# Kernel tuning notes

Hardware: AMD Instinct MI355X
Metric: run time of the kernel (lower is better)

Reference implementation:

```python
import jax, jax.numpy as jnp
import numpy as np

B, T, D = 4, 512, 512
NB, NH, PF, K = 2, 8, 2, 4
INNER = PF * D          # 1024
DH = INNER // NH        # 128
NC = 1000
EPS = 1e-5


def _ln(x, s, b):
    mu = x.mean(-1, keepdims=True)
    var = x.var(-1, keepdims=True)
    return (x - mu) / jnp.sqrt(var + EPS) * s + b


def _causal_conv(x, k, b):
    # x: [B,T,C], depthwise kernel k: [C,K]
    kk = k.shape[-1]
    xp = jnp.pad(x, ((0, 0), (kk - 1, 0), (0, 0)))
    t = x.shape[1]
    y = sum(xp[:, j:j + t, :] * k[:, j] for j in range(kk))
    return y + b


def _mlstm_scan(q, k, v, ip, fp):
    # q,k,v: [B,T,NH,DH]; ip,fp: [B,T,NH]
    b, t, nh, dh = q.shape
    C0 = jnp.zeros((b, nh, dh, dh), q.dtype)
    n0 = jnp.zeros((b, nh, dh), q.dtype)
    m0 = jnp.zeros((b, nh), q.dtype)

    def step(carry, xs):
        C, n, m = carry
        qt, kt, vt, ipt, fpt = xs
        fl = jax.nn.log_sigmoid(fpt)
        m_new = jnp.maximum(fl + m, ipt)
        i = jnp.exp(ipt - m_new)
        f = jnp.exp(fl + m - m_new)
        C = f[..., None, None] * C + i[..., None, None] * (vt[..., :, None] * kt[..., None, :])
        n = f[..., None] * n + i[..., None] * kt
        denom = jnp.maximum(jnp.abs(jnp.einsum('bhd,bhd->bh', n, qt)), 1.0)
        h = jnp.einsum('bhij,bhj->bhi', C, qt) / denom[..., None]
        return (C, n, m_new), h

    tm = lambda a: jnp.swapaxes(a, 0, 1)  # time-major
    _, h = jax.lax.scan(step, (C0, n0, m0), (tm(q), tm(k), tm(v), tm(ip), tm(fp)))
    return jnp.swapaxes(h, 0, 1)  # [B,T,NH,DH]


def _block(x, ln_s, ln_b, w_up, b_up, conv_k, conv_b, w_q, w_k, w_v,
           w_ig, b_ig, w_fg, b_fg, hn_s, w_down, b_down):
    b, t, d = x.shape
    xn = _ln(x, ln_s, ln_b)
    up = xn @ w_up + b_up                       # [B,T,2*INNER]
    xu, z = up[..., :INNER], up[..., INNER:]
    xc = jax.nn.silu(_causal_conv(xu, conv_k, conv_b))
    q = (xc @ w_q).reshape(b, t, NH, DH)
    k = (xc @ w_k).reshape(b, t, NH, DH) * (DH ** -0.5)
    v = (xu @ w_v).reshape(b, t, NH, DH)
    ip = xc @ w_ig + b_ig                       # [B,T,NH]
    fp = xc @ w_fg + b_fg
    h = _mlstm_scan(q, k, v, ip, fp)            # [B,T,NH,DH]
    mu = h.mean(-1, keepdims=True)
    var = h.var(-1, keepdims=True)
    h = (h - mu) / jnp.sqrt(var + EPS) * hn_s   # per-head norm, hn_s: [NH,DH]
    h = h.reshape(b, t, INNER) * jax.nn.silu(z)
    return x + h @ w_down + b_down


def setup_inputs() -> dict:
    key = jax.random.key(0)
    ks = jax.random.split(key, 24)
    g = lambda i, sh, sc: jax.random.normal(ks[i], sh, jnp.float32) * sc
    inp = {
        'x': g(0, (B, T, D), 1.0),
        'cls_token': g(1, (1, 1, D), 0.02),
        'ln_s': jnp.ones((NB, D)), 'ln_b': jnp.zeros((NB, D)),
        'w_up': g(2, (NB, D, 2 * INNER), D ** -0.5), 'b_up': jnp.zeros((NB, 2 * INNER)),
        'conv_k': g(3, (NB, INNER, K), 0.3), 'conv_b': jnp.zeros((NB, INNER)),
        'w_q': g(4, (NB, INNER, INNER), INNER ** -0.5),
        'w_k': g(5, (NB, INNER, INNER), INNER ** -0.5),
        'w_v': g(6, (NB, INNER, INNER), INNER ** -0.5),
        'w_ig': g(7, (NB, INNER, NH), INNER ** -0.5), 'b_ig': jnp.zeros((NB, NH)),
        'w_fg': g(8, (NB, INNER, NH), INNER ** -0.5),
        'b_fg': jnp.full((NB, NH), 3.0),
        'hn_s': jnp.ones((NB, NH, DH)),
        'w_down': g(9, (NB, INNER, D), INNER ** -0.5), 'b_down': jnp.zeros((NB, D)),
        'fc_ln_s': jnp.ones((D,)), 'fc_ln_b': jnp.zeros((D,)),
        'fc_w': g(10, (D, NC), D ** -0.5), 'fc_b': jnp.zeros((NC,)),
    }
    return inp


def reference(x, cls_token, ln_s, ln_b, w_up, b_up, conv_k, conv_b, w_q, w_k, w_v,
              w_ig, b_ig, w_fg, b_fg, hn_s, w_down, b_down,
              fc_ln_s, fc_ln_b, fc_w, fc_b):
    b = x.shape[0]
    # append class token at the last position ('last')
    h = jnp.concatenate([x, jnp.broadcast_to(cls_token, (b, 1, x.shape[-1]))], axis=1)
    for i in range(NB):
        h = _block(h, ln_s[i], ln_b[i], w_up[i], b_up[i], conv_k[i], conv_b[i],
                   w_q[i], w_k[i], w_v[i], w_ig[i], b_ig[i], w_fg[i], b_fg[i],
                   hn_s[i], w_down[i], b_down[i])
    cls = h[:, -1, :]
    y = jax.nn.relu(_ln(cls, fc_ln_s, fc_ln_b)) @ fc_w + fc_b
    return y
```

## Files before the change

kernel.cpp:

```cpp
#include <hip/hip_runtime.h>

#define EPSV 1e-5f
constexpr int Bsz = 4, T0 = 512, Dm = 512, TT = 513, NHh = 8, KK = 4;
constexpr int IN = 1024, DHd = 128, NCc = 1000;
constexpr int ROWS = Bsz * TT;
constexpr int NCH = 9;

constexpr size_t WT_UP = 0;
constexpr size_t WT_Q  = WT_UP + 2048 * 512;
constexpr size_t WT_K  = WT_Q + 1024 * 1024;
constexpr size_t WT_V  = WT_K + 1024 * 1024;
constexpr size_t WT_DN = WT_V + 1024 * 1024;
constexpr size_t WT_STRIDE = WT_DN + 512 * 1024;

typedef __attribute__((ext_vector_type(8))) short bf16x8;
typedef __attribute__((ext_vector_type(4))) float f32x4;
typedef __attribute__((ext_vector_type(4))) unsigned short ushort4v;
typedef __attribute__((ext_vector_type(8))) unsigned short ushort8v;
typedef unsigned short u16;

__device__ __forceinline__ float siluf(float x) { return x / (1.f + __expf(-x)); }
__device__ __forceinline__ u16 f2bf(float f) {
    unsigned int u = __float_as_uint(f);
    u = (u + 0x7FFFu + ((u >> 16) & 1u)) >> 16;
    return (u16)u;
}
__device__ __forceinline__ float bfu(u16 u) {
    return __uint_as_float(((unsigned int)u) << 16);
}

__global__ __launch_bounds__(256) void concat_kernel(const float* __restrict__ x,
                                                     const float* __restrict__ cls,
                                                     float* __restrict__ h) {
    int idx = blockIdx.x * 256 + threadIdx.x;
    if (idx >= Bsz * TT * Dm) return;
    int d = idx & (Dm - 1);
    int bt = idx >> 9;
    int t = bt % TT, b = bt / TT;
    h[idx] = (t < T0) ? x[((size_t)(b * T0 + t)) * Dm + d] : cls[d];
}

__global__ __launch_bounds__(256) void ln_kernel(const float* __restrict__ in,
                                                 const float* __restrict__ s,
                                                 const float* __restrict__ bb,
                                                 u16* __restrict__ out16) {
    int row = blockIdx.x, tid = threadIdx.x;
    const float* r = in + (size_t)row * Dm;
    __shared__ float s1[4], s2[4];
    float x0 = r[tid], x1 = r[tid + 256];
    float sum = x0 + x1, sq = x0 * x0 + x1 * x1;
#pragma unroll
    for (int o = 32; o > 0; o >>= 1) { sum += __shfl_xor(sum, o); sq += __shfl_xor(sq, o); }
    if ((tid & 63) == 0) { s1[tid >> 6] = sum; s2[tid >> 6] = sq; }
    __syncthreads();
    sum = s1[0] + s1[1] + s1[2] + s1[3];
    sq  = s2[0] + s2[1] + s2[2] + s2[3];
    float mu = sum / Dm, var = sq / Dm - mu * mu, inv = rsqrtf(var + EPSV);
    out16[(size_t)row * Dm + tid]       = f2bf((x0 - mu) * inv * s[tid] + bb[tid]);
    out16[(size_t)row * Dm + tid + 256] = f2bf((x1 - mu) * inv * s[tid + 256] + bb[tid + 256]);
}

__global__ __launch_bounds__(256) void w_transpose_kernel(const float* __restrict__ wup,
        const float* __restrict__ wq, const float* __restrict__ wk,
        const float* __restrict__ wv, const float* __restrict__ wdn,
        u16* __restrict__ wt) {
    int y = blockIdx.y;
    int blk = y / 5, sel = y - blk * 5;
    int Kd, N; const float* src; size_t doff;
    if (sel == 0)      { Kd = 512;  N = 2048; src = wup + (size_t)blk * 512 * 2048; doff = WT_UP; }
    else if (sel == 1) { Kd = 1024; N = 1024; src = wq  + (size_t)blk * 1024 * 1024; doff = WT_Q; }
    else if (sel == 2) { Kd = 1024; N = 1024; src = wk  + (size_t)blk * 1024 * 1024; doff = WT_K; }
    else if (sel == 3) { Kd = 1024; N = 1024; src = wv  + (size_t)blk * 1024 * 1024; doff = WT_V; }
    else               { Kd = 1024; N = 512;  src = wdn + (size_t)blk * 1024 * 512;  doff = WT_DN; }
    u16* dst = wt + (size_t)blk * WT_STRIDE + doff;
    int ntx = N >> 5;
    int ntiles = ntx * (Kd >> 5);
    int ti = blockIdx.x;
    if (ti >= ntiles) return;
    int tk = ti / ntx, tn = ti - tk * ntx;
    __shared__ u16 s[32][33];
    int tx = threadIdx.x & 31, ty = threadIdx.x >> 5;
#pragma unroll
    for (int i = 0; i < 4; i++) {
        int k = tk * 32 + ty + i * 8;
        s[ty + i * 8][tx] = f2bf(src[(size_t)k * N + tn * 32 + tx]);
    }
    __syncthreads();
#pragma unroll
    for (int i = 0; i < 4; i++) {
        int n = tn * 32 + ty + i * 8;
        dst[(size_t)n * Kd + tk * 32 + tx] = s[tx][ty + i * 8];
    }
}

template<int BM, int BN>
__device__ __forceinline__ void gemm_tile_body(const u16* __restrict__ A, int lda,
                                               const u16* __restrict__ Wt, int Kd,
                                               const float* __restrict__ bias,
                                               const float* __restrict__ resid, int ldr,
                                               float* __restrict__ Cout, int ldc,
                                               int M, float scale, int m0, int n0,
                                               u16 (*As)[BM][40], u16 (*Bs)[BN][40]) {
    constexpr int MT = BM / 32;
    constexpr int NT = BN / 32;
    constexpr int ANV = BM / 64;
    constexpr int BNV = BN / 64;
    int tid = threadIdx.x;
    int wave = tid >> 6, lane = tid & 63;
    int wm = (wave >> 1) * (BM / 2), wn = (wave & 1) * (BN / 2);
    int lrow = lane & 15, lquad = lane >> 4;

    f32x4 acc[MT][NT];
#pragma unroll
    for (int i = 0; i < MT; i++)
#pragma unroll
        for (int j = 0; j < NT; j++)
#pragma unroll
            for (int r = 0; r < 4; r++) acc[i][j][r] = 0.f;

    int am, ak, bn, bk;
    if (BM == 128) { am = tid >> 1; ak = (tid & 1) * 16; }
    else           { am = tid >> 2; ak = (tid & 3) * 8; }
    if (BN == 128) { bn = tid & 127; bk = (tid >> 7) * 16; }
    else           { bn = tid & 63;  bk = (tid >> 6) * 8; }
    int gm = m0 + am;
    const u16* arow = A + (size_t)(gm < M ? gm : 0) * lda + ak;
    bool avalid = gm < M;
    const u16* wrow = Wt + (size_t)(n0 + bn) * Kd + bk;

    ushort8v areg[ANV];
    ushort8v breg[BNV];

    auto load_tile = [&](int k0) {
        if (avalid) {
#pragma unroll
            for (int i = 0; i < ANV; i++) areg[i] = *(const ushort8v*)(arow + k0 + i * 8);
        } else {
#pragma unroll
            for (int i = 0; i < ANV; i++) areg[i] = (ushort8v){0,0,0,0,0,0,0,0};
        }
#pragma unroll
        for (int i = 0; i < BNV; i++) breg[i] = *(const ushort8v*)(wrow + k0 + i * 8);
    };
    auto store_tile = [&](int buf) {
#pragma unroll
        for (int i = 0; i < ANV; i++)
            *(ushort8v*)&As[buf][am][ak + i * 8] = areg[i];
#pragma unroll
        for (int i = 0; i < BNV; i++)
            *(ushort8v*)&Bs[buf][bn][bk + i * 8] = breg[i];
    };

    load_tile(0);
    store_tile(0);
    __syncthreads();

    int nk = Kd >> 5;
#pragma unroll 1
    for (int it = 0; it < nk; it++) {
        int cur = it & 1;
        bool more = (it + 1 < nk);
        if (more) load_tile((it + 1) << 5);
        bf16x8 afr[MT], bfr[NT];
#pragma unroll
        for (int mt = 0; mt < MT; mt++)
            afr[mt] = *(const bf16x8*)&As[cur][wm + mt * 16 + lrow][lquad * 8];
#pragma unroll
        for (int nt = 0; nt < NT; nt++)
            bfr[nt] = *(const bf16x8*)&Bs[cur][wn + nt * 16 + lrow][lquad * 8];
#pragma unroll
        for (int mt = 0; mt < MT; mt++)
#pragma unroll
            for (int nt = 0; nt < NT; nt++)
                acc[mt][nt] = __builtin_amdgcn_mfma_f32_16x16x32_bf16(
                    afr[mt], bfr[nt], acc[mt][nt], 0, 0, 0);
        if (more) store_tile(cur ^ 1);
        __syncthreads();
    }

#pragma unroll
    for (int mt = 0; mt < MT; mt++) {
#pragma unroll
        for (int r = 0; r < 4; r++) {
            int gmr = m0 + wm + mt * 16 + lquad * 4 + r;
            if (gmr >= M) continue;
#pragma unroll
            for (int nt = 0; nt < NT; nt++) {
                int gn = n0 + wn + nt * 16 + lrow;
                float v = acc[mt][nt][r] * scale;
                if (bias) v += bias[gn];
                if (resid) v += resid[(size_t)gmr * ldr + gn];
                Cout[(size_t)gmr * ldc + gn] = v;
            }
        }
    }
}

template<int BM, int BN>
__global__ __launch_bounds__(256, 2) void gemm_mfma_kernel(const u16* __restrict__ A, int lda,
                                                           const u16* __restrict__ Wt, int Kd,
                                                           const float* __restrict__ bias,
                                                           const float* __restrict__ resid, int ldr,
                                                           float* __restrict__ Cout, int ldc,
                                                           int M, float scale) {
    __shared__ __align__(16) u16 As[2][BM][40];
    __shared__ __align__(16) u16 Bs[2][BN][40];
    gemm_tile_body<BM, BN>(A, lda, Wt, Kd, bias, resid, ldr, Cout, ldc, M, scale,
                           blockIdx.y * BM, blockIdx.x * BN, As, Bs);
}

__global__ __launch_bounds__(256, 2) void qkv_mfma_kernel(const u16* __restrict__ xc16,
                                                          const u16* __restrict__ xu16,
                                                          const u16* __restrict__ wtblk,
                                                          float* __restrict__ fq,
                                                          float* __restrict__ fk,
                                                          float* __restrict__ fv,
                                                          float kscale) {
    __shared__ __align__(16) u16 As[2][128][40];
    __shared__ __align__(16) u16 Bs[2][64][40];
    int sel = blockIdx.x >> 4, nx = blockIdx.x & 15;
    const u16* A = (sel == 2) ? xu16 : xc16;
    const u16* Wt = wtblk + ((sel == 0) ? WT_Q : (sel == 1) ? WT_K : WT_V);
    float* C = (sel == 0) ? fq : (sel == 1) ? fk : fv;
    float scale = (sel == 1) ? kscale : 1.f;
    gemm_tile_body<128, 64>(A, IN, Wt, IN, nullptr, nullptr, 0, C, IN, ROWS, scale,
                            blockIdx.y * 128, nx * 64, As, Bs);
}

__global__ __launch_bounds__(256) void conv_silu_kernel(const float* __restrict__ up,
                                                        const float* __restrict__ ck,
                                                        const float* __restrict__ cb,
                                                        float* __restrict__ xc,
                                                        u16* __restrict__ xc16,
                                                        u16* __restrict__ xu16) {
    int idx = blockIdx.x * 256 + threadIdx.x;
    if (idx >= ROWS * IN) return;
    int c = idx & (IN - 1);
    int bt = idx >> 10;
    int t = bt % TT, b = bt / TT;
    float cur = up[((size_t)(b * TT + t)) * (2 * IN) + c];
    float acc = cb[c] + cur * ck[c * KK + (KK - 1)];
#pragma unroll
    for (int j = 0; j < KK - 1; j++) {
        int tt = t - (KK - 1) + j;
        if (tt >= 0) acc += up[((size_t)(b * TT + tt)) * (2 * IN) + c] * ck[c * KK + j];
    }
    float s = siluf(acc);
    xc[idx] = s;
    xc16[idx] = f2bf(s);
    xu16[idx] = f2bf(cur);
}

__global__ __launch_bounds__(256) void gate_w_transpose(const float* __restrict__ wig,
                                                        const float* __restrict__ wfg,
                                                        float* __restrict__ wt) {
    int idx = blockIdx.x * 256 + threadIdx.x;
    int k = idx & 1023;
    int g = (idx >> 10) & 15;
    int blk = idx >> 14;
    const float* w = (g < 8) ? (wig + (size_t)blk * IN * NHh) : (wfg + (size_t)blk * IN * NHh);
    wt[idx] = w[k * NHh + (g & 7)];
}

__global__ __launch_bounds__(256) void gates_kernel(const float* __restrict__ xc,
                                                    const float* __restrict__ wt,
                                                    const float* __restrict__ big,
                                                    const float* __restrict__ bfg,
                                                    float* __restrict__ ip, float* __restrict__ fp) {
    int row = blockIdx.x, tid = threadIdx.x;
    __shared__ float sx[IN];
    *(float4*)&sx[tid * 4] = *(const float4*)(xc + (size_t)row * IN + tid * 4);
    __syncthreads();
    int g = tid >> 4, l = tid & 15;
    const float* wrow = wt + g * IN;
    float acc = 0.f;
#pragma unroll
    for (int j = 0; j < 16; j++) {
        int k = j * 64 + l * 4;
        float4 w4 = *(const float4*)(wrow + k);
        float4 x4 = *(const float4*)&sx[k];
        acc += w4.x * x4.x + w4.y * x4.y + w4.z * x4.z + w4.w * x4.w;
    }
#pragma unroll
    for (int o = 8; o > 0; o >>= 1) acc += __shfl_down(acc, o, 16);
    if (l == 0) {
        if (g < 8) ip[(size_t)row * NHh + g] = acc + big[g];
        else       fp[(size_t)row * NHh + (g - 8)] = acc + bfg[g - 8];
    }
}

__global__ __launch_bounds__(64) void gate_scan_kernel(const float* __restrict__ ip,
        const float* __restrict__ fp, float* __restrict__ gG, float* __restrict__ gM,
        float* __restrict__ gMb, float* __restrict__ gDec) {
    constexpr int PER = 9;
    int chain = blockIdx.x;
    int b = chain >> 3, h = chain & 7;
    int lane = threadIdx.x;
    int tbase = lane * PER;
    float lcs[PER];
    float gi[PER];
    float csum = 0.f;
#pragma unroll
    for (int i = 0; i < PER; i++) {
        int t = tbase + i;
        float fpv = 0.f, ipv = 0.f;
        if (t < TT) {
            size_t gidx = (size_t)(b * TT + t) * NHh + h;
            fpv = fp[gidx]; ipv = ip[gidx];
        }
        float flv = (fpv >= 0.f) ? -log1pf(__expf(-fpv)) : (fpv - log1pf(__expf(fpv)));
        if (t >= TT) flv = 0.f;
        csum += flv;
        lcs[i] = csum;
        gi[i] = ipv;
    }
    float ps = csum;
#pragma unroll
    for (int o = 1; o < 64; o <<= 1) {
        float v = __shfl_up(ps, o);
        if (lane >= o) ps += v;
    }
    float Fexcl = ps - csum;
    float G[PER];
    float cmax = -1e30f;
#pragma unroll
    for (int i = 0; i < PER; i++) {
        int t = tbase + i;
        G[i] = (t < TT) ? (gi[i] - (Fexcl + lcs[i])) : -1e30f;
        cmax = fmaxf(cmax, G[i]);
        lcs[i] = cmax;
    }
    float pm = cmax;
#pragma unroll
    for (int o = 1; o < 64; o <<= 1) {
        float v = __shfl_up(pm, o);
        if (lane >= o) pm = fmaxf(pm, v);
    }
    float Me = __shfl_up(pm, 1);
    if (lane == 0) Me = -1e30f;
    __shared__ float sMb[NCH];
#pragma unroll
    for (int i = 0; i < PER; i++) {
        int t = tbase + i;
        if (t < TT) {
            float Mt = fmaxf(0.f, fmaxf(Me, lcs[i]));
            gG[chain * TT + t] = G[i];
            gM[chain * TT + t] = Mt;
            if (((t & 63) == 63) || t == TT - 1) sMb[t >> 6] = Mt;
        }
    }
    __syncthreads();
    if (lane < NCH) {
        float Mb = sMb[lane];
        float Mbp = (lane == 0) ? 0.f : sMb[lane - 1];
        gMb[chain * NCH + lane] = Mb;
        gDec[chain * NCH + lane] = __expf(Mbp - Mb);
    }
}

__global__ __launch_bounds__(256, 2) void chunk_state_kernel(const float* __restrict__ kk,
        const float* __restrict__ vv, const float* __restrict__ gG,
        const float* __restrict__ gMb, float* __restrict__ P, float* __restrict__ nP) {
    int c = blockIdx.x, chain = blockIdx.y;
    int b = chain >> 3, h = chain & 7;
    int t0 = c * 64;
    int nvalid = min(64, TT - t0);
    __shared__ __align__(16) u16 sWv[128][72];
    __shared__ __align__(16) u16 sKt[128][72];
    __shared__ float sw[64];
    int tid = threadIdx.x;
    if (tid < 64) {
        float Mb = gMb[chain * NCH + c];
        sw[tid] = (tid < nvalid) ? __expf(gG[chain * TT + t0 + tid] - Mb) : 0.f;
    }
    __syncthreads();

    {
        int j = tid >> 2, d0 = (tid & 3) * 32;
        bool val = j < nvalid;
        float wj = sw[j];
        size_t gb = ((size_t)(b * TT + t0 + j)) * IN + h * DHd + d0;
#pragma unroll
        for (int i = 0; i < 8; i++) {
            float4 k4 = val ? *(const float4*)(kk + gb + i * 4) : make_float4(0.f, 0.f, 0.f, 0.f);
            float4 v4 = val ? *(const float4*)(vv + gb + i * 4) : make_float4(0.f, 0.f, 0.f, 0.f);
            int dd = d0 + i * 4;
            int jc = j ^ (((dd >> 5) & 3) << 4);
            sKt[dd + 0][jc] = f2bf(k4.x);
            sKt[dd + 1][jc] = f2bf(k4.y);
            sKt[dd + 2][jc] = f2bf(k4.z);
            sKt[dd + 3][jc] = f2bf(k4.w);
            sWv[dd + 0][jc] = f2bf(v4.x * wj);
            sWv[dd + 1][jc] = f2bf(v4.y * wj);
            sWv[dd + 2][jc] = f2bf(v4.z * wj);
            sWv[dd + 3][jc] = f2bf(v4.w * wj);
        }
    }
    __syncthreads();

    int wave = tid >> 6, lane = tid & 63;
    int lrow = lane & 15, lquad = lane >> 4;
    int wm = (wave >> 1) * 64, wn = (wave & 1) * 64;
    f32x4 acc[4][4];
#pragma unroll
    for (int mt = 0; mt < 4; mt++)
#pragma unroll
        for (int nt = 0; nt < 4; nt++)
#pragma unroll
            for (int r = 0; r < 4; r++) acc[mt][nt][r] = 0.f;

#pragma unroll
    for (int ks = 0; ks < 2; ks++) {
        bf16x8 af[4], bfr[4];
#pragma unroll
        for (int mt = 0; mt < 4; mt++) {
            int r = wm + mt * 16 + lrow;
            int g = (ks * 4 + lquad) ^ (((r >> 5) & 3) << 1);
            af[mt] = *(const bf16x8*)&sWv[r][g * 8];
        }
#pragma unroll
        for (int nt = 0; nt < 4; nt++) {
            int r = wn + nt * 16 + lrow;
            int g = (ks * 4 + lquad) ^ (((r >> 5) & 3) << 1);
            bfr[nt] = *(const bf16x8*)&sKt[r][g * 8];
        }
#pragma unroll
        for (int mt = 0; mt < 4; mt++)
#pragma unroll
            for (int nt = 0; nt < 4; nt++)
                acc[mt][nt] = __builtin_amdgcn_mfma_f32_16x16x32_bf16(
                    af[mt], bfr[nt], acc[mt][nt], 0, 0, 0);
    }

    float* Pbase = P + (((size_t)(c * 32 + chain)) << 14);
#pragma unroll
    for (int mt = 0; mt < 4; mt++)
#pragma unroll
        for (int r = 0; r < 4; r++) {
            int e = wm + mt * 16 + lquad * 4 + r;
#pragma unroll
            for (int nt = 0; nt < 4; nt++) {
                int d = wn + nt * 16 + lrow;
                Pbase[(size_t)e * 128 + d] = acc[mt][nt][r];
            }
        }

    {
        int d = tid >> 1, jh = (tid & 1) * 32;
        int swz = ((d >> 5) & 3) << 4;
        float an = 0.f;
#pragma unroll
        for (int j = 0; j < 32; j++) {
            int jj = jh + j;
            an += sw[jj] * bfu(sKt[d][jj ^ swz]);
        }
        an += __shfl_xor(an, 1);
        if ((tid & 1) == 0) nP[(size_t)(c * 32 + chain) * 128 + d] = an;
    }
}

__global__ __launch_bounds__(256) void chunk_combine_kernel(float* __restrict__ P,
        const float* __restrict__ gDec) {
    int chain = blockIdx.x >> 6;
    int idx = (blockIdx.x & 63) * 256 + threadIdx.x;
    float run = 0.f;
    for (int c = 0; c < NCH; c++) {
        size_t a = (((size_t)(c * 32 + chain)) << 14) + idx;
        float tmp = P[a];
        P[a] = run;
        run = run * gDec[chain * NCH + c] + tmp;
    }
}

__global__ __launch_bounds__(256) void n_combine_kernel(float* __restrict__ nP,
        const float* __restrict__ gDec) {
    int gidx = blockIdx.x * 256 + threadIdx.x;
    int chain = gidx >> 7, d = gidx & 127;
    float run = 0.f;
    for (int c = 0; c < NCH; c++) {
        size_t a = (size_t)(c * 32 + chain) * 128 + d;
        float tmp = nP[a];
        nP[a] = run;
        run = run * gDec[chain * NCH + c] + tmp;
    }
}

__global__ __launch_bounds__(512, 2) void chunk_out_kernel(const float* __restrict__ qq,
        const float* __restrict__ kk, const float* __restrict__ vv,
        const float* __restrict__ gG, const float* __restrict__ gM,
        const float* __restrict__ gMb, const float* __restrict__ P,
        const float* __restrict__ nP, float* __restrict__ hs) {
    int c = blockIdx.x, chain = blockIdx.y;
    int b = chain >> 3, h = chain & 7;
    int t0 = c * 64;
    int nvalid = min(64, TT - t0);
    __shared__ __align__(16) u16 smem[30720];
    __shared__ float sG[64], sM[64], sWr[64], sInv[64], sNb[128], sRS[2][64];
    u16* sQ  = smem;
    u16* sCB = smem + 8704;
    u16* sK  = smem + 8704;
    u16* sVt = smem;
    u16* sD  = smem + 26112;
    int tid = threadIdx.x;
    int wave = tid >> 6, lane = tid & 63;
    int lrow = lane & 15, lquad = lane >> 4;
    int mq = wave >> 1, nh = wave & 1;

    float Mbprev = (c > 0) ? gMb[chain * NCH + c - 1] : 0.f;
    if (tid < 64) {
        bool val = tid < nvalid;
        sG[tid] = val ? gG[chain * TT + t0 + tid] : -1e30f;
        float Mv = val ? gM[chain * TT + t0 + tid] : 1e30f;
        sM[tid] = Mv;
        sWr[tid] = val ? __expf(Mbprev - Mv) : 0.f;
    }
    if (tid >= 128 && tid < 256) sNb[tid - 128] = nP[(size_t)(c * 32 + chain) * 128 + (tid - 128)];

    {
        int lr = tid >> 3, c0 = (tid & 7) * 16;
        bool val = lr < nvalid;
        size_t gb = ((size_t)(b * TT + t0 + lr)) * IN + h * DHd + c0;
#pragma unroll
        for (int i = 0; i < 4; i++) {
            float4 q4 = val ? *(const float4*)(qq + gb + i * 4) : make_float4(0.f,0.f,0.f,0.f);
            ushort4v tq = {f2bf(q4.x), f2bf(q4.y), f2bf(q4.z), f2bf(q4.w)};
            *(ushort4v*)&sQ[lr * 136 + c0 + i * 4] = tq;
        }
    }
    {
        const float* CBbase = P + (((size_t)(c * 32 + chain)) << 14);
        int e = tid >> 2, d0 = (tid & 3) * 32;
#pragma unroll
        for (int i = 0; i < 8; i++) {
            float4 c4 = *(const float4*)(CBbase + (size_t)e * 128 + d0 + i * 4);
            ushort4v tc = {f2bf(c4.x), f2bf(c4.y), f2bf(c4.z), f2bf(c4.w)};
            *(ushort4v*)&sCB[e * 136 + d0 + i * 4] = tc;
        }
    }
    __syncthreads();

    f32x4 acc[4];
#pragma unroll
    for (int tt = 0; tt < 4; tt++)
#pragma unroll
        for (int r = 0; r < 4; r++) acc[tt][r] = 0.f;
#pragma unroll 1
    for (int ks = 0; ks < 4; ks++) {
        bf16x8 af = *(const bf16x8*)&sQ[(mq * 16 + lrow) * 136 + ks * 32 + lquad * 8];
#pragma unroll
        for (int tt = 0; tt < 4; tt++) {
            bf16x8 bf = *(const bf16x8*)&sCB[(nh * 64 + tt * 16 + lrow) * 136 + ks * 32 + lquad * 8];
            acc[tt] = __builtin_amdgcn_mfma_f32_16x16x32_bf16(af, bf, acc[tt], 0, 0, 0);
        }
    }
#pragma unroll
    for (int tt = 0; tt < 4; tt++)
#pragma unroll
        for (int r = 0; r < 4; r++) acc[tt][r] *= sWr[mq * 16 + lquad * 4 + r];
    __syncthreads();

    {
        int lr = tid >> 3, c0 = (tid & 7) * 16;
        bool val = lr < nvalid;
        size_t gb = ((size_t)(b * TT + t0 + lr)) * IN + h * DHd + c0;
#pragma unroll
        for (int i = 0; i < 4; i++) {
            float4 k4 = val ? *(const float4*)(kk + gb + i * 4) : make_float4(0.f,0.f,0.f,0.f);
            ushort4v tk = {f2bf(k4.x), f2bf(k4.y), f2bf(k4.z), f2bf(k4.w)};
            *(ushort4v*)&sK[lr * 136 + c0 + i * 4] = tk;
        }
    }
    __syncthreads();

    {
        f32x4 accS[2];
#pragma unroll
        for (int tt = 0; tt < 2; tt++)
#pragma unroll
            for (int r = 0; r < 4; r++) accS[tt][r] = 0.f;
#pragma unroll 1
        for (int ks = 0; ks < 4; ks++) {
            bf16x8 af = *(const bf16x8*)&sQ[(mq * 16 + lrow) * 136 + ks * 32 + lquad * 8];
#pragma unroll
            for (int tt = 0; tt < 2; tt++) {
                bf16x8 bf = *(const bf16x8*)&sK[((nh * 2 + tt) * 16 + lrow) * 136 + ks * 32 + lquad * 8];
                accS[tt] = __builtin_amdgcn_mfma_f32_16x16x32_bf16(af, bf, accS[tt], 0, 0, 0);
            }
        }
        float rsum[4] = {0.f, 0.f, 0.f, 0.f};
#pragma unroll
        for (int tt = 0; tt < 2; tt++) {
            int j = (nh * 2 + tt) * 16 + lrow;
            float Gj = sG[j];
#pragma unroll
            for (int r = 0; r < 4; r++) {
                int t = mq * 16 + lquad * 4 + r;
                float w = (j <= t) ? __expf(Gj - sM[t]) : 0.f;
                float wD = accS[tt][r] * w;
                rsum[r] += wD;
                sD[t * 72 + j] = f2bf(wD);
            }
        }
#pragma unroll
        for (int r = 0; r < 4; r++) {
#pragma unroll
            for (int msk = 1; msk < 16; msk <<= 1) rsum[r] += __shfl_xor(rsum[r], msk);
        }
        if (lrow == 0) {
#pragma unroll
            for (int r = 0; r < 4; r++) sRS[nh][mq * 16 + lquad * 4 + r] = rsum[r];
        }
    }
    __syncthreads();

    if (tid < 64) {
        float qn = 0.f;
#pragma unroll 1
        for (int d4 = 0; d4 < 32; d4++) {
            ushort4v q4 = *(const ushort4v*)&sQ[tid * 136 + d4 * 4];
            float4 nb = *(const float4*)&sNb[d4 * 4];
            qn += bfu(q4.x) * nb.x + bfu(q4.y) * nb.y + bfu(q4.z) * nb.z + bfu(q4.w) * nb.w;
        }
        float den = sRS[0][tid] + sRS[1][tid] + sWr[tid] * qn;
        sInv[tid] = 1.f / fmaxf(fabsf(den), 1.f);
    }
    __syncthreads();

    {
        int e = tid & 127, tg = (tid >> 7) * 16;
#pragma unroll 1
        for (int i = 0; i < 16; i++) {
            int t = tg + i;
            float v = (t < nvalid) ? vv[((size_t)(b * TT + t0 + t)) * IN + h * DHd + e] : 0.f;
            sVt[e * 72 + t] = f2bf(v);
        }
    }
    __syncthreads();

#pragma unroll 1
    for (int ks = 0; ks < 2; ks++) {
        bf16x8 af = *(const bf16x8*)&sD[(mq * 16 + lrow) * 72 + ks * 32 + lquad * 8];
#pragma unroll
        for (int tt = 0; tt < 4; tt++) {
            bf16x8 bf = *(const bf16x8*)&sVt[(nh * 64 + tt * 16 + lrow) * 72 + ks * 32 + lquad * 8];
            acc[tt] = __builtin_amdgcn_mfma_f32_16x16x32_bf16(af, bf, acc[tt], 0, 0, 0);
        }
    }

#pragma unroll
    for (int tt = 0; tt < 4; tt++) {
#pragma unroll
        for (int r = 0; r < 4; r++) {
            int t = mq * 16 + lquad * 4 + r;
            if (t < nvalid) {
                int e = nh * 64 + tt * 16 + lrow;
                hs[((size_t)(b * TT + t0 + t)) * IN + h * DHd + e] = acc[tt][r] * sInv[t];
            }
        }
    }
}

__global__ __launch_bounds__(64) void headnorm_kernel(const float* __restrict__ hs,
                                                      const float* __restrict__ hn,
                                                      const float* __restrict__ up,
                                                      u16* __restrict__ out16) {
    int idx = blockIdx.x;
    int h = idx & 7, bt = idx >> 3;
    int tid = threadIdx.x;
    size_t base = (size_t)bt * IN + h * DHd;
    float x0 = hs[base + tid], x1 = hs[base + 64 + tid];
    float sum = x0 + x1, sq = x0 * x0 + x1 * x1;
#pragma unroll
    for (int o = 32; o > 0; o >>= 1) { sum += __shfl_xor(sum, o); sq += __shfl_xor(sq, o); }
    float mu = sum / DHd, var = sq / DHd - mu * mu, inv = rsqrtf(var + EPSV);
    size_t zb = (size_t)bt * (2 * IN) + IN + h * DHd;
    out16[base + tid]      = f2bf((x0 - mu) * inv * hn[h * DHd + tid]      * siluf(up[zb + tid]));
    out16[base + 64 + tid] = f2bf((x1 - mu) * inv * hn[h * DHd + 64 + tid] * siluf(up[zb + 64 + tid]));
}

__global__ __launch_bounds__(256) void cls_ln_kernel(const float* __restrict__ hbuf,
                                                     const float* __restrict__ s, const float* __restrict__ bb,
                                                     float* __restrict__ vcls) {
    int b = blockIdx.x, tid = threadIdx.x;
    const float* r = hbuf + ((size_t)b * TT + TT - 1) * Dm;
    __shared__ float s1[4], s2[4];
    float x0 = r[tid], x1 = r[tid + 256];
    float sum = x0 + x1, sq = x0 * x0 + x1 * x1;
#pragma unroll
    for (int o = 32; o > 0; o >>= 1) { sum += __shfl_xor(sum, o); sq += __shfl_xor(sq, o); }
    if ((tid & 63) == 0) { s1[tid >> 6] = sum; s2[tid >> 6] = sq; }
    __syncthreads();
    sum = s1[0] + s1[1] + s1[2] + s1[3];
    sq  = s2[0] + s2[1] + s2[2] + s2[3];
    float mu = sum / Dm, var = sq / Dm - mu * mu, inv = rsqrtf(var + EPSV);
    float n0 = (x0 - mu) * inv * s[tid] + bb[tid];
    float n1 = (x1 - mu) * inv * s[tid + 256] + bb[tid + 256];
    vcls[b * Dm + tid]       = fmaxf(n0, 0.f);
    vcls[b * Dm + tid + 256] = fmaxf(n1, 0.f);
}

__global__ __launch_bounds__(256) void fc_kernel(const float* __restrict__ vcls,
                                                 const float* __restrict__ fw,
                                                 const float* __restrict__ fb,
                                                 float* __restrict__ out) {
    __shared__ float svc[Bsz][Dm];
    __shared__ float sred[4][256];
    int tid = threadIdx.x;
    int j0 = blockIdx.x * 64;
    {
        const float4* src = (const float4*)vcls;
        float4* dst = (float4*)&svc[0][0];
        dst[tid] = src[tid];
        dst[tid + 256] = src[tid + 256];
    }
    __syncthreads();
    int j = j0 + (tid & 63);
    int chunk = tid >> 6;
    int kbase = chunk * 128;
    float a0 = 0.f, a1 = 0.f, a2 = 0.f, a3 = 0.f;
    if (j < NCc) {
        const float* fwp = fw + (size_t)kbase * NCc + j;
#pragma unroll 4
        for (int kk = 0; kk < 128; kk++) {
            float w = fwp[(size_t)kk * NCc];
            a0 += svc[0][kbase + kk] * w;
            a1 += svc[1][kbase + kk] * w;
            a2 += svc[2][kbase + kk] * w;
            a3 += svc[3][kbase + kk] * w;
        }
    }
    int jl = tid & 63;
    sred[chunk][jl * 4 + 0] = a0;
    sred[chunk][jl * 4 + 1] = a1;
    sred[chunk][jl * 4 + 2] = a2;
    sred[chunk][jl * 4 + 3] = a3;
    __syncthreads();
    if (tid < 64) {
        int jj = j0 + tid;
        if (jj < NCc) {
            float bias = fb[jj];
#pragma unroll
            for (int b = 0; b < Bsz; b++) {
                float v = sred[0][tid * 4 + b] + sred[1][tid * 4 + b]
                        + sred[2][tid * 4 + b] + sred[3][tid * 4 + b];
                out[b * NCc + jj] = v + bias;
            }
        }
    }
}

extern "C" void kernel_launch(void* const* d_in, const int* in_sizes, int n_in,
                              void* d_out, int out_size, void* d_ws, size_t ws_size,
                              hipStream_t stream) {
    const float* x      = (const float*)d_in[0];
    const float* cls    = (const float*)d_in[1];
    const float* ln_s   = (const float*)d_in[2];
    const float* ln_b   = (const float*)d_in[3];
    const float* w_up   = (const float*)d_in[4];
    const float* b_up   = (const float*)d_in[5];
    const float* conv_k = (const float*)d_in[6];
    const float* conv_b = (const float*)d_in[7];
    const float* w_q    = (const float*)d_in[8];
    const float* w_k    = (const float*)d_in[9];
    const float* w_v    = (const float*)d_in[10];
    const float* w_ig   = (const float*)d_in[11];
    const float* b_ig   = (const float*)d_in[12];
    const float* w_fg   = (const float*)d_in[13];
    const float* b_fg   = (const float*)d_in[14];
    const float* hn_s   = (const float*)d_in[15];
    const float* w_down = (const float*)d_in[16];
    const float* b_down = (const float*)d_in[17];
    const float* fcls   = (const float*)d_in[18];
    const float* fclb   = (const float*)d_in[19];
    const float* fc_w   = (const float*)d_in[20];
    const float* fc_b   = (const float*)d_in[21];
    float* out = (float*)d_out;

    float* ws = (float*)d_ws;
    size_t off = 0;
    float* f_h  = ws + off; off += (size_t)ROWS * Dm;
    float* f_up = ws + off; off += (size_t)ROWS * 2 * IN;
    float* f_xc = ws + off; off += (size_t)ROWS * IN;
    float* f_q  = ws + off; off += (size_t)ROWS * IN;
    float* f_k  = ws + off; off += (size_t)ROWS * IN;
    float* f_v  = ws + off; off += (size_t)ROWS * IN;
    float* f_hs = ws + off; off += (size_t)ROWS * IN;
    float* f_ip = ws + off; off += (size_t)ROWS * NHh;
    float* f_fp = ws + off; off += (size_t)ROWS * NHh;
    float* g_G  = ws + off; off += 32 * TT;
    float* g_M  = ws + off; off += 32 * TT;
    float* g_Mb = ws + off; off += 32 * NCH;
    float* g_De = ws + off; off += 32 * NCH;
    float* g_P  = ws + off; off += (size_t)NCH * 32 * DHd * DHd;
    float* g_nP = ws + off; off += (size_t)NCH * 32 * DHd;
    float* f_vc = ws + off; off += Bsz * Dm;
    float* g_wt = ws + off; off += 2 * 16 * IN;
    u16* g_Wt  = (u16*)(ws + off); off += (2 * WT_STRIDE + 1) / 2;
    u16* f_xn16 = (u16*)(ws + off); off += ((size_t)ROWS * Dm + 1) / 2;
    u16* f_xc16 = (u16*)(ws + off); off += ((size_t)ROWS * IN + 1) / 2;
    u16* f_xu16 = (u16*)(ws + off); off += ((size_t)ROWS * IN + 1) / 2;
    u16* f_xg16 = (u16*)(ws + off); off += ((size_t)ROWS * IN + 1) / 2;

    const float kscale = 0.08838834764831845f;
    const int MB = (ROWS + 127) / 128;
    const int MB64 = (ROWS + 63) / 64;

    concat_kernel<<<(ROWS * Dm + 255) / 256, 256, 0, stream>>>(x, cls, f_h);
    gate_w_transpose<<<(2 * 16 * IN + 255) / 256, 256, 0, stream>>>(w_ig, w_fg, g_wt);
    w_transpose_kernel<<<dim3(1024, 10), 256, 0, stream>>>(w_up, w_q, w_k, w_v, w_down, g_Wt);

    for (int blk = 0; blk < 2; blk++) {
        const float* p_ln_s = ln_s + blk * Dm;
        const float* p_ln_b = ln_b + blk * Dm;
        const float* p_bup  = b_up + (size_t)blk * 2 * IN;
        const float* p_ck   = conv_k + (size_t)blk * IN * KK;
        const float* p_cb   = conv_b + (size_t)blk * IN;
        const float* p_big  = b_ig + (size_t)blk * NHh;
        const float* p_bfg  = b_fg + (size_t)blk * NHh;
        const float* p_hns  = hn_s + (size_t)blk * NHh * DHd;
        const float* p_bd   = b_down + (size_t)blk * Dm;
        const u16*   p_wt   = g_Wt + (size_t)blk * WT_STRIDE;

        ln_kernel<<<ROWS, 256, 0, stream>>>(f_h, p_ln_s, p_ln_b, f_xn16);

        gemm_mfma_kernel<128, 64><<<dim3(2 * IN / 64, MB), 256, 0, stream>>>(
            f_xn16, Dm, p_wt + WT_UP, Dm, p_bup, nullptr, 0, f_up, 2 * IN, ROWS, 1.f);

        conv_silu_kernel<<<(ROWS * IN + 255) / 256, 256, 0, stream>>>(
            f_up, p_ck, p_cb, f_xc, f_xc16, f_xu16);

        qkv_mfma_kernel<<<dim3(48, MB), 256, 0, stream>>>(
            f_xc16, f_xu16, p_wt, f_q, f_k, f_v, kscale);

        gates_kernel<<<ROWS, 256, 0, stream>>>(f_xc, g_wt + blk * 16 * IN, p_big, p_bfg,
                                               f_ip, f_fp);

        gate_scan_kernel<<<32, 64, 0, stream>>>(f_ip, f_fp, g_G, g_M, g_Mb, g_De);
        chunk_state_kernel<<<dim3(NCH, 32), 256, 0, stream>>>(f_k, f_v, g_G, g_Mb, g_P, g_nP);
        chunk_combine_kernel<<<32 * 64, 256, 0, stream>>>(g_P, g_De);
        n_combine_kernel<<<16, 256, 0, stream>>>(g_nP, g_De);
        chunk_out_kernel<<<dim3(NCH, 32), 512, 0, stream>>>(f_q, f_k, f_v, g_G, g_M, g_Mb,
                                                            g_P, g_nP, f_hs);

        headnorm_kernel<<<ROWS * NHh, 64, 0, stream>>>(f_hs, p_hns, f_up, f_xg16);

        gemm_mfma_kernel<64, 64><<<dim3(Dm / 64, MB64), 256, 0, stream>>>(
            f_xg16, IN, p_wt + WT_DN, IN, p_bd, f_h, Dm, f_h, Dm, ROWS, 1.f);
    }

    cls_ln_kernel<<<Bsz, 256, 0, stream>>>(f_h, fcls, fclb, f_vc);
    fc_kernel<<<(NCc + 63) / 64, 256, 0, stream>>>(f_vc, fc_w, fc_b, out);
}
```

Before: 460.6 us.

## Use direct global-to-LDS loads with 128x128 tiles for up and QKV GEMMs

Adds a new GEMM body for the up-projection and fused QKV projections. It uses `global_load_lds` to copy bf16 A and W tiles straight from global memory into shared memory, skipping the register staging step. Tiles grow to 128x128 with 64x64 per-wave MFMA sub-tiles. The bf16 activation buffers are padded to a multiple of 128 rows, so out-of-range rows can be loaded without bounds checks. In exchange, the loop is single-buffered with two barriers per k-step, which gives up load/compute overlap, and the unpadded LDS rows may cause bank conflicts.

After: 451.6 us. About the same (-1.9%).

```diff
diff --git a/kernel.cpp b/kernel.cpp
--- a/kernel.cpp
+++ b/kernel.cpp
@@ -4,6 +4,7 @@
 constexpr int Bsz = 4, T0 = 512, Dm = 512, TT = 513, NHh = 8, KK = 4;
 constexpr int IN = 1024, DHd = 128, NCc = 1000;
 constexpr int ROWS = Bsz * TT;
+constexpr int MPAD = 2176;
 constexpr int NCH = 9;
 
 constexpr size_t WT_UP = 0;
@@ -27,6 +28,11 @@
 }
 __device__ __forceinline__ float bfu(u16 u) {
     return __uint_as_float(((unsigned int)u) << 16);
+}
+__device__ __forceinline__ void gload16(const u16* g, u16* l) {
+    __builtin_amdgcn_global_load_lds(
+        (const __attribute__((address_space(1))) void*)g,
+        (__attribute__((address_space(3))) void*)l, 16, 0, 0);
 }
 
 __global__ __launch_bounds__(256) void concat_kernel(const float* __restrict__ x,
@@ -209,22 +215,100 @@
                            blockIdx.y * BM, blockIdx.x * BN, As, Bs);
 }
 
-__global__ __launch_bounds__(256, 2) void qkv_mfma_kernel(const u16* __restrict__ xc16,
-                                                          const u16* __restrict__ xu16,
-                                                          const u16* __restrict__ wtblk,
-                                                          float* __restrict__ fq,
-                                                          float* __restrict__ fk,
-                                                          float* __restrict__ fv,
-                                                          float kscale) {
-    __shared__ __align__(16) u16 As[2][128][40];
-    __shared__ __align__(16) u16 Bs[2][64][40];
-    int sel = blockIdx.x >> 4, nx = blockIdx.x & 15;
+__device__ __forceinline__ void gemm128_body(const u16* __restrict__ A, int lda,
+                                             const u16* __restrict__ Wt, int Kd,
+                                             const float* __restrict__ bias,
+                                             float* __restrict__ Cout, int ldc,
+                                             int M, float scale, int m0, int n0,
+                                             u16* As, u16* Bs) {
+    int tid = threadIdx.x;
+    int wave = tid >> 6, lane = tid & 63;
+    int lrow = lane & 15, lquad = lane >> 4;
+    int wm = (wave >> 1) * 64, wn = (wave & 1) * 64;
+
+    const u16* ag0 = A + (size_t)(m0 + wave * 16 + (lane >> 2)) * lda + (lane & 3) * 8;
+    const u16* ag1 = ag0 + (size_t)64 * lda;
+    const u16* bg0 = Wt + (size_t)(n0 + wave * 16 + (lane >> 2)) * Kd + (lane & 3) * 8;
+    const u16* bg1 = bg0 + (size_t)64 * Kd;
+    u16* la0 = As + wave * 512;
+    u16* la1 = As + 2048 + wave * 512;
+    u16* lb0 = Bs + wave * 512;
+    u16* lb1 = Bs + 2048 + wave * 512;
+
+    f32x4 acc[4][4];
+#pragma unroll
+    for (int i = 0; i < 4; i++)
+#pragma unroll
+        for (int j = 0; j < 4; j++)
+#pragma unroll
+            for (int r = 0; r < 4; r++) acc[i][j][r] = 0.f;
+
+    int nk = Kd >> 5;
+#pragma unroll 1
+    for (int it = 0; it < nk; it++) {
+        int k0 = it << 5;
+        gload16(ag0 + k0, la0);
+        gload16(ag1 + k0, la1);
+        gload16(bg0 + k0, lb0);
+        gload16(bg1 + k0, lb1);
+        __syncthreads();
+        bf16x8 afr[4], bfr[4];
+#pragma unroll
+        for (int mt = 0; mt < 4; mt++)
+            afr[mt] = *(const bf16x8*)&As[(wm + mt * 16 + lrow) * 32 + lquad * 8];
+#pragma unroll
+        for (int nt = 0; nt < 4; nt++)
+            bfr[nt] = *(const bf16x8*)&Bs[(wn + nt * 16 + lrow) * 32 + lquad * 8];
+#pragma unroll
+        for (int mt = 0; mt < 4; mt++)
+#pragma unroll
+            for (int nt = 0; nt < 4; nt++)
+                acc[mt][nt] = __builtin_amdgcn_mfma_f32_16x16x32_bf16(
+                    afr[mt], bfr[nt], acc[mt][nt], 0, 0, 0);
+        __syncthreads();
+    }
+
+#pragma unroll
+    for (int mt = 0; mt < 4; mt++) {
+#pragma unroll
+        for (int r = 0; r < 4; r++) {
+            int gmr = m0 + wm + mt * 16 + lquad * 4 + r;
+            if (gmr >= M) continue;
+#pragma unroll
+            for (int nt = 0; nt < 4; nt++) {
+                int gn = n0 + wn + nt * 16 + lrow;
+                float v = acc[mt][nt][r] * scale;
+                if (bias) v += bias[gn];
+                Cout[(size_t)gmr * ldc + gn] = v;
+            }
+        }
+    }
+}
+
+__global__ __launch_bounds__(256, 2) void up_gl_kernel(const u16* __restrict__ A,
+        const u16* __restrict__ Wt, const float* __restrict__ bias, float* __restrict__ C) {
+    __shared__ __align__(16) u16 As[128 * 32];
+    __shared__ __align__(16) u16 Bs[128 * 32];
+    gemm128_body(A, Dm, Wt, Dm, bias, C, 2 * IN, ROWS, 1.f,
+                 blockIdx.y * 128, blockIdx.x * 128, As, Bs);
+}
+
+__global__ __launch_bounds__(256, 2) void qkv_gl_kernel(const u16* __restrict__ xc16,
+                                                        const u16* __restrict__ xu16,
+                                                        const u16* __restrict__ wtblk,
+                                                        float* __restrict__ fq,
+                                                        float* __restrict__ fk,
+                                                        float* __restrict__ fv,
+                                                        float kscale) {
+    __shared__ __align__(16) u16 As[128 * 32];
+    __shared__ __align__(16) u16 Bs[128 * 32];
+    int sel = blockIdx.x >> 3, nx = blockIdx.x & 7;
     const u16* A = (sel == 2) ? xu16 : xc16;
     const u16* Wt = wtblk + ((sel == 0) ? WT_Q : (sel == 1) ? WT_K : WT_V);
     float* C = (sel == 0) ? fq : (sel == 1) ? fk : fv;
     float scale = (sel == 1) ? kscale : 1.f;
-    gemm_tile_body<128, 64>(A, IN, Wt, IN, nullptr, nullptr, 0, C, IN, ROWS, scale,
-                            blockIdx.y * 128, nx * 64, As, Bs);
+    gemm128_body(A, IN, Wt, IN, nullptr, C, IN, ROWS, scale,
+                 blockIdx.y * 128, nx * 128, As, Bs);
 }
 
 __global__ __launch_bounds__(256) void conv_silu_kernel(const float* __restrict__ up,
@@ -796,9 +880,9 @@
     float* f_vc = ws + off; off += Bsz * Dm;
     float* g_wt = ws + off; off += 2 * 16 * IN;
     u16* g_Wt  = (u16*)(ws + off); off += (2 * WT_STRIDE + 1) / 2;
-    u16* f_xn16 = (u16*)(ws + off); off += ((size_t)ROWS * Dm + 1) / 2;
-    u16* f_xc16 = (u16*)(ws + off); off += ((size_t)ROWS * IN + 1) / 2;
-    u16* f_xu16 = (u16*)(ws + off); off += ((size_t)ROWS * IN + 1) / 2;
+    u16* f_xn16 = (u16*)(ws + off); off += ((size_t)MPAD * Dm) / 2;
+    u16* f_xc16 = (u16*)(ws + off); off += ((size_t)MPAD * IN) / 2;
+    u16* f_xu16 = (u16*)(ws + off); off += ((size_t)MPAD * IN) / 2;
     u16* f_xg16 = (u16*)(ws + off); off += ((size_t)ROWS * IN + 1) / 2;
 
     const float kscale = 0.08838834764831845f;
@@ -823,13 +907,13 @@
 
         ln_kernel<<<ROWS, 256, 0, stream>>>(f_h, p_ln_s, p_ln_b, f_xn16);
 
-        gemm_mfma_kernel<128, 64><<<dim3(2 * IN / 64, MB), 256, 0, stream>>>(
-            f_xn16, Dm, p_wt + WT_UP, Dm, p_bup, nullptr, 0, f_up, 2 * IN, ROWS, 1.f);
+        up_gl_kernel<<<dim3(2 * IN / 128, MB), 256, 0, stream>>>(
+            f_xn16, p_wt + WT_UP, p_bup, f_up);
 
         conv_silu_kernel<<<(ROWS * IN + 255) / 256, 256, 0, stream>>>(
             f_up, p_ck, p_cb, f_xc, f_xc16, f_xu16);
 
-        qkv_mfma_kernel<<<dim3(48, MB), 256, 0, stream>>>(
+        qkv_gl_kernel<<<dim3(24, MB), 256, 0, stream>>>(
             f_xc16, f_xu16, p_wt, f_q, f_k, f_v, kscale);
 
         gates_kernel<<<ROWS, 256, 0, stream>>>(f_xc, g_wt + blk * 16 * IN, p_big, p_bfg,
```
